# Kernel tuning notes

Hardware: AMD Instinct MI355X
Metric: run time of the kernel (lower is better)

## Reference

```python
import jax, jax.numpy as jnp
import numpy as np


def setup_inputs() -> dict:
    key = jax.random.key(0)
    k1, k2, k3, k4, k5 = jax.random.split(key, 5)
    B, N, M, K, D, O = 4, 32768, 8192, 16, 64, 64
    x = jax.random.normal(k1, (B, N, D), jnp.float32)
    x_subset = jax.random.normal(k2, (B, M, D), jnp.float32)
    knn_index = jax.random.randint(k3, (B, M, K), 0, N, jnp.int32)
    # 1x1 Conv2d(2*D -> O) == per-point linear: weight (O, 2D), bias (O,)
    W = jax.random.normal(k4, (O, 2 * D), jnp.float32) * (1.0 / np.sqrt(2 * D))
    b = jax.random.normal(k5, (O,), jnp.float32) * 0.01
    return {"x": x, "x_subset": x_subset, "knn_index": knn_index, "W": W, "b": b}


def reference(x, x_subset, knn_index, W, b):
    # knn_gather: (B,N,D) indexed by (B,M,K) -> (B,M,K,D)
    grouped = jax.vmap(lambda xb, ib: xb[ib])(x, knn_index)
    center = x_subset[:, :, None, :]                      # (B,M,1,D)
    edge = jnp.concatenate(
        [grouped - center, jnp.broadcast_to(center, grouped.shape)], axis=-1
    )                                                     # (B,M,K,2D)
    # 1x1 conv over channel dim + ReLU, output layout (B,O,M,K)
    h = jax.nn.relu(jnp.einsum("bmkc,oc->bomk", edge, W) + b[None, :, None, None])
    return jnp.max(h, axis=-1)                            # (B,O,M)
```

## Files before the change

kernel.cpp:

```cpp
#include <hip/hip_runtime.h>
#include <math.h>

#define B_ 4
#define N_ 32768
#define M_ 8192
#define K_ 16
#define D_ 64
#define O_ 64

typedef __attribute__((ext_vector_type(8))) short bf16x8;
typedef __attribute__((ext_vector_type(4))) float f32x4;

static __device__ __forceinline__ short f2bf(float f) {
    unsigned u = __float_as_uint(f);
    u += 0x7fffu + ((u >> 16) & 1u);
    return (short)(u >> 16);
}

static __device__ __forceinline__ bf16x8 ld_bf8(const float* p) {
    float4 f0 = *(const float4*)p;
    float4 f1 = *(const float4*)(p + 4);
    bf16x8 v;
    v[0] = f2bf(f0.x); v[1] = f2bf(f0.y); v[2] = f2bf(f0.z); v[3] = f2bf(f0.w);
    v[4] = f2bf(f1.x); v[5] = f2bf(f1.y); v[6] = f2bf(f1.z); v[7] = f2bf(f1.w);
    return v;
}

__global__ __launch_bounds__(256)
void fused_gconv(const float* __restrict__ x, const float* __restrict__ xs,
                 const int* __restrict__ idx, const float* __restrict__ W,
                 const float* __restrict__ bias, float* __restrict__ out) {
    __shared__ int   ldsI[64 * 16];
    __shared__ float ldsT[64 * 65];

    const int tid  = threadIdx.x;
    const int blk  = blockIdx.x;
    const int bb   = blk >> 7;
    const int mblk = (blk & 127) * 64;

    *(int4*)&ldsI[tid * 4] =
        *(const int4*)(idx + ((size_t)bb * M_ + mblk) * 16 + tid * 4);

    const int l  = tid & 63;
    const int wv = tid >> 6;
    const int lr = l & 15;
    const int kg = l >> 4;
    const int mw = wv * 16;

    bf16x8 b1[2][4], bd[2][4];
    float  binit[4];
    #pragma unroll
    for (int t = 0; t < 4; ++t) {
        #pragma unroll
        for (int s = 0; s < 2; ++s) {
            const float* wp = W + (size_t)(t * 16 + lr) * 128 + s * 32 + kg * 8;
            float4 f0 = *(const float4*)wp;
            float4 f1 = *(const float4*)(wp + 4);
            float4 g0 = *(const float4*)(wp + 64);
            float4 g1 = *(const float4*)(wp + 68);
            bf16x8 v1, vd;
            v1[0] = f2bf(f0.x); v1[1] = f2bf(f0.y); v1[2] = f2bf(f0.z); v1[3] = f2bf(f0.w);
            v1[4] = f2bf(f1.x); v1[5] = f2bf(f1.y); v1[6] = f2bf(f1.z); v1[7] = f2bf(f1.w);
            vd[0] = f2bf(g0.x - f0.x); vd[1] = f2bf(g0.y - f0.y);
            vd[2] = f2bf(g0.z - f0.z); vd[3] = f2bf(g0.w - f0.w);
            vd[4] = f2bf(g1.x - f1.x); vd[5] = f2bf(g1.y - f1.y);
            vd[6] = f2bf(g1.z - f1.z); vd[7] = f2bf(g1.w - f1.w);
            b1[s][t] = v1;
            bd[s][t] = vd;
        }
        binit[t] = bias[t * 16 + lr];
    }

    const float* xsp = xs + ((size_t)bb * M_ + mblk + mw + lr) * 64 + kg * 8;
    bf16x8 axs0 = ld_bf8(xsp);
    bf16x8 axs1 = ld_bf8(xsp + 32);

    float vout[4][4];
    #pragma unroll
    for (int t = 0; t < 4; ++t) {
        f32x4 a = {binit[t], binit[t], binit[t], binit[t]};
        a = __builtin_amdgcn_mfma_f32_16x16x32_bf16(axs0, bd[0][t], a, 0, 0, 0);
        a = __builtin_amdgcn_mfma_f32_16x16x32_bf16(axs1, bd[1][t], a, 0, 0, 0);
        vout[t][0] = a[0]; vout[t][1] = a[1];
        vout[t][2] = a[2]; vout[t][3] = a[3];
    }

    __syncthreads();

    const float* xb = x + (size_t)bb * N_ * 64;

    #pragma unroll
    for (int m = 0; m < 16; ++m) {
        const int rr = ldsI[(mw + m) * 16 + lr];
        const float* xp = xb + (size_t)(unsigned)rr * 64 + kg * 8;
        bf16x8 a0 = ld_bf8(xp);
        bf16x8 a1 = ld_bf8(xp + 32);
        #pragma unroll
        for (int t = 0; t < 4; ++t) {
            f32x4 a = {0.f, 0.f, 0.f, 0.f};
            a = __builtin_amdgcn_mfma_f32_16x16x32_bf16(a0, b1[0][t], a, 0, 0, 0);
            a = __builtin_amdgcn_mfma_f32_16x16x32_bf16(a1, b1[1][t], a, 0, 0, 0);
            float v = fmaxf(fmaxf(a[0], a[1]), fmaxf(a[2], a[3]));
            v = fmaxf(v, __shfl_xor(v, 16));
            v = fmaxf(v, __shfl_xor(v, 32));
            if ((m >> 2) == kg)
                vout[t][m & 3] += v;
        }
    }

    #pragma unroll
    for (int t = 0; t < 4; ++t)
        #pragma unroll
        for (int r = 0; r < 4; ++r) {
            float v = vout[t][r];
            ldsT[(t * 16 + lr) * 65 + mw + kg * 4 + r] = v > 0.f ? v : 0.f;
        }
    __syncthreads();

    const int o  = tid >> 2;
    const int ms = (tid & 3) * 16;
    float* op = out + ((size_t)bb * 64 + o) * M_ + mblk + ms;
    #pragma unroll
    for (int j = 0; j < 4; ++j) {
        const float* lp = &ldsT[o * 65 + ms + j * 4];
        *(float4*)(op + j * 4) = make_float4(lp[0], lp[1], lp[2], lp[3]);
    }
}

extern "C" void kernel_launch(void* const* d_in, const int* in_sizes, int n_in,
                              void* d_out, int out_size, void* d_ws, size_t ws_size,
                              hipStream_t stream) {
    const float* x    = (const float*)d_in[0];
    const float* xs   = (const float*)d_in[1];
    const int*   idx  = (const int*)d_in[2];
    const float* W    = (const float*)d_in[3];
    const float* bias = (const float*)d_in[4];
    float* out = (float*)d_out;

    fused_gconv<<<(B_ * M_) / 64, 256, 0, stream>>>(x, xs, idx, W, bias, out);
}
```

Baseline: 33.02 us.

## Shrink blocks to 16 centers and map batches to XCDs for L2 locality

Each block now handles 16 center points instead of 64, so the grid has four times as many blocks. Each wave gathers 4 centers' neighbors with no masked accumulation. Block indices are remapped so each XCD (blk&7) serves one half of one batch, keeping that batch's gathered x rows in the same L2. The cost is more redundant weight loads and bf16 conversion per block, plus per-block setup overhead.

```diff
diff --git a/kernel.cpp b/kernel.cpp
--- a/kernel.cpp
+++ b/kernel.cpp
@@ -30,22 +30,22 @@
 void fused_gconv(const float* __restrict__ x, const float* __restrict__ xs,
                  const int* __restrict__ idx, const float* __restrict__ W,
                  const float* __restrict__ bias, float* __restrict__ out) {
-    __shared__ int   ldsI[64 * 16];
-    __shared__ float ldsT[64 * 65];
+    __shared__ int   ldsI[256];
+    __shared__ float ldsT[64 * 17];
 
     const int tid  = threadIdx.x;
     const int blk  = blockIdx.x;
-    const int bb   = blk >> 7;
-    const int mblk = (blk & 127) * 64;
+    const int xcd  = blk & 7;
+    const int slot = blk >> 3;
+    const int bb   = xcd >> 1;
+    const int m0   = (((xcd & 1) << 8) + slot) << 4;
 
-    *(int4*)&ldsI[tid * 4] =
-        *(const int4*)(idx + ((size_t)bb * M_ + mblk) * 16 + tid * 4);
+    ldsI[tid] = idx[((size_t)bb * M_ + m0) * 16 + tid];
 
     const int l  = tid & 63;
     const int wv = tid >> 6;
     const int lr = l & 15;
     const int kg = l >> 4;
-    const int mw = wv * 16;
 
     bf16x8 b1[2][4], bd[2][4];
     float  binit[4];
@@ -71,27 +71,26 @@
         binit[t] = bias[t * 16 + lr];
     }
 
-    const float* xsp = xs + ((size_t)bb * M_ + mblk + mw + lr) * 64 + kg * 8;
+    const float* xsp = xs + ((size_t)bb * M_ + m0 + lr) * 64 + kg * 8;
     bf16x8 axs0 = ld_bf8(xsp);
     bf16x8 axs1 = ld_bf8(xsp + 32);
-
-    float vout[4][4];
+    f32x4 cacc[4];
     #pragma unroll
     for (int t = 0; t < 4; ++t) {
         f32x4 a = {binit[t], binit[t], binit[t], binit[t]};
         a = __builtin_amdgcn_mfma_f32_16x16x32_bf16(axs0, bd[0][t], a, 0, 0, 0);
         a = __builtin_amdgcn_mfma_f32_16x16x32_bf16(axs1, bd[1][t], a, 0, 0, 0);
-        vout[t][0] = a[0]; vout[t][1] = a[1];
-        vout[t][2] = a[2]; vout[t][3] = a[3];
+        cacc[t] = a;
     }
 
     __syncthreads();
 
     const float* xb = x + (size_t)bb * N_ * 64;
 
+    float gmax[4][4];
     #pragma unroll
-    for (int m = 0; m < 16; ++m) {
-        const int rr = ldsI[(mw + m) * 16 + lr];
+    for (int j = 0; j < 4; ++j) {
+        const int rr = ldsI[(wv * 4 + j) * 16 + lr];
         const float* xp = xb + (size_t)(unsigned)rr * 64 + kg * 8;
         bf16x8 a0 = ld_bf8(xp);
         bf16x8 a1 = ld_bf8(xp + 32);
@@ -103,28 +102,26 @@
             float v = fmaxf(fmaxf(a[0], a[1]), fmaxf(a[2], a[3]));
             v = fmaxf(v, __shfl_xor(v, 16));
             v = fmaxf(v, __shfl_xor(v, 32));
-            if ((m >> 2) == kg)
-                vout[t][m & 3] += v;
+            gmax[t][j] = v;
         }
     }
 
-    #pragma unroll
-    for (int t = 0; t < 4; ++t)
+    if (kg == wv) {
         #pragma unroll
-        for (int r = 0; r < 4; ++r) {
-            float v = vout[t][r];
-            ldsT[(t * 16 + lr) * 65 + mw + kg * 4 + r] = v > 0.f ? v : 0.f;
-        }
+        for (int t = 0; t < 4; ++t)
+            #pragma unroll
+            for (int r = 0; r < 4; ++r) {
+                float v = gmax[t][r] + cacc[t][r];
+                ldsT[(t * 16 + lr) * 17 + wv * 4 + r] = v > 0.f ? v : 0.f;
+            }
+    }
     __syncthreads();
 
     const int o  = tid >> 2;
-    const int ms = (tid & 3) * 16;
-    float* op = out + ((size_t)bb * 64 + o) * M_ + mblk + ms;
-    #pragma unroll
-    for (int j = 0; j < 4; ++j) {
-        const float* lp = &ldsT[o * 65 + ms + j * 4];
-        *(float4*)(op + j * 4) = make_float4(lp[0], lp[1], lp[2], lp[3]);
-    }
+    const int mj = (tid & 3) * 4;
+    const float* lp = &ldsT[o * 17 + mj];
+    float4 v = make_float4(lp[0], lp[1], lp[2], lp[3]);
+    *(float4*)(out + ((size_t)bb * 64 + o) * M_ + m0 + mj) = v;
 }
 
 extern "C" void kernel_launch(void* const* d_in, const int* in_sizes, int n_in,
@@ -137,5 +134,5 @@
     const float* bias = (const float*)d_in[4];
     float* out = (float*)d_out;
 
-    fused_gconv<<<(B_ * M_) / 64, 256, 0, stream>>>(x, xs, idx, W, bias, out);
+    fused_gconv<<<(B_ * M_) / 16, 256, 0, stream>>>(x, xs, idx, W, bias, out);
 }
```

Measured after the change: 54.99 us. 1.67x slower.
